# Kernel optimization log

Hardware: AMD Instinct MI355X
Metric: run time of the kernel (lower is better)

The kernel has to match this reference:

```python
import jax, jax.numpy as jnp
import numpy as np

BS, T, H = 4, 2048, 512
N_HEAD = 8
D_HEAD = H // N_HEAD  # 64


def setup_inputs() -> dict:
    key = jax.random.key(0)
    k1, k2, k3 = jax.random.split(key, 3)
    x = jax.random.normal(k1, (BS, T, H), dtype=jnp.float32)
    # torch Linear(hidden, (2*n_head+1)*d_head) -> store transposed for x @ W
    w_qkv = jax.random.normal(k2, (H, (2 * N_HEAD + 1) * D_HEAD), dtype=jnp.float32) * (H ** -0.5)
    w_out = jax.random.normal(k3, (D_HEAD, H), dtype=jnp.float32) * (D_HEAD ** -0.5)
    return {"x": x, "w_qkv": w_qkv, "w_out": w_out}


def reference(x, w_qkv, w_out):
    bs, t, h = x.shape
    n_head, d_head = N_HEAD, D_HEAD
    scale = d_head ** -0.5

    qkv = x @ w_qkv  # [bs, t, (2*n_head+1)*d_head]
    q, k, v = jnp.split(qkv, [n_head * d_head, 2 * n_head * d_head], axis=-1)
    q = q.reshape(bs, t, n_head, d_head)
    k = k.reshape(bs, t, n_head, d_head)
    # v stays [bs, t, d_head]: a single V shared across all heads

    # causal mask: -inf strictly above the diagonal
    mask = jnp.triu(jnp.full((t, t), -jnp.inf, dtype=x.dtype), 1)

    # scores: [bs, n_head, t_q, t_k]
    attn_score = jnp.einsum('bqhd,bkhd->bhqk', q, k) * scale + mask
    attn_prob = jax.nn.softmax(attn_score, axis=-1)

    # shared V broadcast over heads: [bs, n_head, t, d_head]
    attn_vec = jnp.einsum('bhqk,bkd->bhqd', attn_prob, v)
    m_attn_vec = jnp.mean(attn_vec, axis=1)  # mean over heads -> [bs, t, d_head]

    out = m_attn_vec @ w_out  # [bs, t, hidden]
    return out, attn_prob
```

## Files before the change

### kernel.cpp

```cpp
#include <hip/hip_runtime.h>

typedef unsigned short u16;
typedef __bf16 bf16x8 __attribute__((ext_vector_type(8)));
typedef float f32x4 __attribute__((ext_vector_type(4)));
static_assert(sizeof(bf16x8) == 16, "bf16x8 must be 16B");

#define MFMA(a, b, c) __builtin_amdgcn_mfma_f32_16x16x32_bf16(a, b, c, 0, 0, 0)

__device__ __forceinline__ u16 f2bf(float f) {
  unsigned u = __float_as_uint(f);
  u += 0x7fffu + ((u >> 16) & 1u);
  return (u16)(u >> 16);
}

__global__ __launch_bounds__(256) void prep_kernel(
    const float* __restrict__ x, const float* __restrict__ wqkv,
    const float* __restrict__ wout, u16* __restrict__ xh,
    u16* __restrict__ wt, u16* __restrict__ wot) {
  int blk = blockIdx.x, tid = threadIdx.x;
  if (blk < 4096) {
    int idx = (blk * 256 + tid) * 4;
    float4 v = *(const float4*)(x + idx);
    ushort4 o;
    o.x = f2bf(v.x); o.y = f2bf(v.y); o.z = f2bf(v.z); o.w = f2bf(v.w);
    *(ushort4*)(xh + idx) = o;
  } else if (blk < 4096 + 2176) {
    int idx = (blk - 4096) * 256 + tid;
    int n = idx >> 9, k = idx & 511;
    float v = wqkv[k * 1088 + n];
    if (n < 512) v *= 0.125f;
    wt[idx] = f2bf(v);
  } else {
    int idx = (blk - 6272) * 256 + tid;
    int n = idx >> 6, d = idx & 63;
    wot[idx] = f2bf(wout[d * 512 + n]);
  }
}

__global__ __launch_bounds__(256) void qkv_gemm_kernel(
    const u16* __restrict__ xh, const u16* __restrict__ wt,
    u16* __restrict__ Qb, u16* __restrict__ Kb, u16* __restrict__ Vt) {
  __shared__ u16 As[128][40];
  __shared__ u16 Bs[64][40];
  const int tid = threadIdx.x;
  const int w = tid >> 6, l = tid & 63, g = l >> 4, c16 = l & 15;
  const int n0 = blockIdx.x * 64;
  const int m0 = blockIdx.y * 128;
  const int arow = tid >> 1, acol = (tid & 1) << 4;
  const int brow = tid >> 2, bcol = (tid & 3) << 3;
  const u16* ap = xh + (size_t)(m0 + arow) * 512 + acol;
  const u16* bp = wt + (size_t)(n0 + brow) * 512 + bcol;
  uint4 pa0 = *(const uint4*)(ap);
  uint4 pa1 = *(const uint4*)(ap + 8);
  uint4 pb0 = *(const uint4*)(bp);
  f32x4 acc[2][4] = {};
  for (int k0 = 0; k0 < 512; k0 += 32) {
    __syncthreads();
    *(uint4*)&As[arow][acol] = pa0;
    *(uint4*)&As[arow][acol + 8] = pa1;
    *(uint4*)&Bs[brow][bcol] = pb0;
    __syncthreads();
    if (k0 + 32 < 512) {
      pa0 = *(const uint4*)(ap + k0 + 32);
      pa1 = *(const uint4*)(ap + k0 + 40);
      pb0 = *(const uint4*)(bp + k0 + 32);
    }
#pragma unroll
    for (int mt = 0; mt < 2; ++mt) {
      bf16x8 a = *(const bf16x8*)&As[w * 32 + mt * 16 + c16][g * 8];
#pragma unroll
      for (int nt = 0; nt < 4; ++nt) {
        bf16x8 b = *(const bf16x8*)&Bs[nt * 16 + c16][g * 8];
        acc[mt][nt] = MFMA(a, b, acc[mt][nt]);
      }
    }
  }
#pragma unroll
  for (int mt = 0; mt < 2; ++mt)
#pragma unroll
    for (int nt = 0; nt < 4; ++nt)
#pragma unroll
      for (int j = 0; j < 4; ++j) {
        u16 bv = f2bf(acc[mt][nt][j]);
        int row = m0 + w * 32 + mt * 16 + g * 4 + j;
        int b = row >> 11, t = row & 2047;
        int col = n0 + nt * 16 + c16;
        if (col < 512) {
          int h = col >> 6, d = col & 63;
          Qb[((size_t)((b << 3) + h) * 2048 + t) * 64 + d] = bv;
        } else if (col < 1024) {
          int cc = col - 512, h = cc >> 6, d = cc & 63;
          Kb[((size_t)((b << 3) + h) * 2048 + t) * 64 + d] = bv;
        } else {
          int d = col - 1024;
          Vt[((size_t)((b << 6) + d)) * 2048 + t] = bv;
        }
      }
}

__global__ __launch_bounds__(256) void attn_kernel(
    const u16* __restrict__ Qb, const u16* __restrict__ Kb,
    const u16* __restrict__ Vt, float* __restrict__ P,
    float* __restrict__ Obuf) {
  __shared__ u16 Ps[64][72];
  __shared__ u16 Ks[2][64][72];
  const int tid = threadIdx.x;
  const int w = tid >> 6, l = tid & 63, g = l >> 4, c16 = l & 15;
  const int bidx = blockIdx.x;
  const int ii = bidx >> 5, jj = bidx & 31;
  const int qt = ((ii >> 3) & 1) ? (31 - jj) : jj;
  const int bh = ii, b = bh >> 3;
  const int srow = tid >> 2, scol = (tid & 3) << 4;

  const u16* qrow = Qb + ((size_t)(bh * 2048 + qt * 64 + w * 16 + c16)) * 64;
  const bf16x8 aq0 = *(const bf16x8*)(qrow + g * 8);
  const bf16x8 aq1 = *(const bf16x8*)(qrow + 32 + g * 8);

  const u16* kb = Kb + ((size_t)bh * 2048) * 64;
  const u16* vb = Vt + ((size_t)(b << 6)) * 2048;

  float lsum = 0.f;

  uint4 ka0 = *(const uint4*)(kb + (size_t)srow * 64 + scol);
  uint4 ka1 = *(const uint4*)(kb + (size_t)srow * 64 + scol + 8);
  for (int kt = 0; kt <= qt; ++kt) {
    const int cur = kt & 1;
    *(uint4*)&Ks[cur][srow][scol] = ka0;
    *(uint4*)&Ks[cur][srow][scol + 8] = ka1;
    if (kt < qt) {
      const u16* kn = kb + (size_t)((kt + 1) * 64 + srow) * 64 + scol;
      ka0 = *(const uint4*)(kn);
      ka1 = *(const uint4*)(kn + 8);
    }
    __syncthreads();
    f32x4 st[4];
    __builtin_amdgcn_s_setprio(1);
#pragma unroll
    for (int nt = 0; nt < 4; ++nt) {
      bf16x8 k0 = *(const bf16x8*)&Ks[cur][nt * 16 + c16][g * 8];
      bf16x8 k1 = *(const bf16x8*)&Ks[cur][nt * 16 + c16][32 + g * 8];
      f32x4 a = {};
      a = MFMA(k0, aq0, a);
      a = MFMA(k1, aq1, a);
      st[nt] = a;
    }
    __builtin_amdgcn_s_setprio(0);
    if (kt == qt) {
#pragma unroll
      for (int nt = 0; nt < 4; ++nt)
#pragma unroll
        for (int j = 0; j < 4; ++j)
          if (nt * 16 + g * 4 + j > w * 16 + c16) st[nt][j] = -3.0e38f;
    }
#pragma unroll
    for (int nt = 0; nt < 4; ++nt)
#pragma unroll
      for (int j = 0; j < 4; ++j) lsum += __expf(st[nt][j]);
  }
  lsum += __shfl_xor(lsum, 16, 64);
  lsum += __shfl_xor(lsum, 32, 64);
  const float rl = 1.0f / lsum;

  __syncthreads();

  f32x4 oacc[4] = {};
  ka0 = *(const uint4*)(kb + (size_t)srow * 64 + scol);
  ka1 = *(const uint4*)(kb + (size_t)srow * 64 + scol + 8);
  float* prow = P +
      ((size_t)(bh * 2048 + qt * 64 + w * 16 + c16)) * 2048 + g * 4;
  for (int kt = 0; kt <= qt; ++kt) {
    const int cur = kt & 1;
    *(uint4*)&Ks[cur][srow][scol] = ka0;
    *(uint4*)&Ks[cur][srow][scol + 8] = ka1;
    if (kt < qt) {
      const u16* kn = kb + (size_t)((kt + 1) * 64 + srow) * 64 + scol;
      ka0 = *(const uint4*)(kn);
      ka1 = *(const uint4*)(kn + 8);
    }
    __syncthreads();
    f32x4 st[4];
    __builtin_amdgcn_s_setprio(1);
#pragma unroll
    for (int nt = 0; nt < 4; ++nt) {
      bf16x8 k0 = *(const bf16x8*)&Ks[cur][nt * 16 + c16][g * 8];
      bf16x8 k1 = *(const bf16x8*)&Ks[cur][nt * 16 + c16][32 + g * 8];
      f32x4 a = {};
      a = MFMA(k0, aq0, a);
      a = MFMA(k1, aq1, a);
      st[nt] = a;
    }
    __builtin_amdgcn_s_setprio(0);
    bf16x8 v0[4], v1[4];
#pragma unroll
    for (int nt = 0; nt < 4; ++nt) {
      const u16* vr = vb + (size_t)(nt * 16 + c16) * 2048 + kt * 64 + g * 8;
      v0[nt] = *(const bf16x8*)(vr);
      v1[nt] = *(const bf16x8*)(vr + 32);
    }
    if (kt == qt) {
#pragma unroll
      for (int nt = 0; nt < 4; ++nt)
#pragma unroll
        for (int j = 0; j < 4; ++j)
          if (nt * 16 + g * 4 + j > w * 16 + c16) st[nt][j] = -3.0e38f;
    }
#pragma unroll
    for (int nt = 0; nt < 4; ++nt) {
      f32x4 pv;
#pragma unroll
      for (int j = 0; j < 4; ++j) pv[j] = __expf(st[nt][j]) * rl;
      __builtin_nontemporal_store(
          pv, (f32x4*)(prow + (size_t)kt * 64 + nt * 16));
      unsigned r0, r1;
      asm("v_cvt_pk_bf16_f32 %0, %1, %2" : "=v"(r0) : "v"(pv[0]), "v"(pv[1]));
      asm("v_cvt_pk_bf16_f32 %0, %1, %2" : "=v"(r1) : "v"(pv[2]), "v"(pv[3]));
      uint2 pk; pk.x = r0; pk.y = r1;
      *(uint2*)&Ps[w * 16 + c16][nt * 16 + g * 4] = pk;
    }
    bf16x8 ap0 = *(const bf16x8*)&Ps[w * 16 + c16][g * 8];
    bf16x8 ap1 = *(const bf16x8*)&Ps[w * 16 + c16][32 + g * 8];
    __builtin_amdgcn_s_setprio(1);
#pragma unroll
    for (int nt = 0; nt < 4; ++nt) {
      oacc[nt] = MFMA(ap0, v0[nt], oacc[nt]);
      oacc[nt] = MFMA(ap1, v1[nt], oacc[nt]);
    }
    __builtin_amdgcn_s_setprio(0);
  }

  {
    float* obase = Obuf + ((size_t)(bh * 2048 + qt * 64 + w * 16)) * 64;
#pragma unroll
    for (int nt = 0; nt < 4; ++nt)
#pragma unroll
      for (int j = 0; j < 4; ++j)
        obase[(g * 4 + j) * 64 + nt * 16 + c16] = oacc[nt][j];
  }
  {
    int colstart = (qt + 1) * 64;
    int nf4 = (2048 - colstart) >> 2;
    float* base = P + ((size_t)(bh * 2048 + qt * 64)) * 2048;
    f32x4 z = {0.f, 0.f, 0.f, 0.f};
    for (int r = 0; r < 64; ++r) {
      f32x4* rowp = (f32x4*)(base + (size_t)r * 2048 + colstart);
      for (int u = tid; u < nf4; u += 256)
        __builtin_nontemporal_store(z, rowp + u);
    }
  }
}

__global__ __launch_bounds__(256) void mean_kernel(
    const float* __restrict__ Obuf, u16* __restrict__ meanb) {
  int o4 = blockIdx.x * 256 + threadIdx.x;
  int d4 = o4 & 15, t = (o4 >> 4) & 2047, b = o4 >> 15;
  f32x4 acc = {0.f, 0.f, 0.f, 0.f};
#pragma unroll
  for (int h = 0; h < 8; ++h) {
    f32x4 v = *(const f32x4*)(Obuf +
        ((size_t)((b << 3) + h) * 2048 + t) * 64 + d4 * 4);
    acc += v;
  }
  ushort4 o;
  o.x = f2bf(acc[0] * 0.125f); o.y = f2bf(acc[1] * 0.125f);
  o.z = f2bf(acc[2] * 0.125f); o.w = f2bf(acc[3] * 0.125f);
  *(ushort4*)(meanb + (size_t)o4 * 4) = o;
}

__global__ __launch_bounds__(256) void out_gemm_kernel(
    const u16* __restrict__ meanb, const u16* __restrict__ wot,
    float* __restrict__ out) {
  __shared__ u16 As[64][72];
  __shared__ u16 Bs[64][72];
  const int tid = threadIdx.x;
  const int w = tid >> 6, l = tid & 63, g = l >> 4, c16 = l & 15;
  const int n0 = blockIdx.x * 64;
  const int m0 = blockIdx.y * 64;
  const int srow = tid >> 2, scol = (tid & 3) << 4;
  {
    const u16* asrc = meanb + (size_t)(m0 + srow) * 64 + scol;
    *(uint4*)&As[srow][scol] = *(const uint4*)(asrc);
    *(uint4*)&As[srow][scol + 8] = *(const uint4*)(asrc + 8);
    const u16* bsrc = wot + (size_t)(n0 + srow) * 64 + scol;
    *(uint4*)&Bs[srow][scol] = *(const uint4*)(bsrc);
    *(uint4*)&Bs[srow][scol + 8] = *(const uint4*)(bsrc + 8);
  }
  __syncthreads();
  bf16x8 a0 = *(const bf16x8*)&As[w * 16 + c16][g * 8];
  bf16x8 a1 = *(const bf16x8*)&As[w * 16 + c16][32 + g * 8];
  f32x4 acc[4] = {};
#pragma unroll
  for (int nt = 0; nt < 4; ++nt) {
    bf16x8 b0 = *(const bf16x8*)&Bs[nt * 16 + c16][g * 8];
    bf16x8 b1 = *(const bf16x8*)&Bs[nt * 16 + c16][32 + g * 8];
    acc[nt] = MFMA(a0, b0, acc[nt]);
    acc[nt] = MFMA(a1, b1, acc[nt]);
  }
#pragma unroll
  for (int nt = 0; nt < 4; ++nt)
#pragma unroll
    for (int j = 0; j < 4; ++j)
      __builtin_nontemporal_store(
          acc[nt][j],
          out + (size_t)(m0 + w * 16 + g * 4 + j) * 512 + n0 + nt * 16 + c16);
}

extern "C" void kernel_launch(void* const* d_in, const int* in_sizes, int n_in,
                              void* d_out, int out_size, void* d_ws,
                              size_t ws_size, hipStream_t stream) {
  (void)in_sizes; (void)n_in; (void)out_size; (void)ws_size;
  const float* x = (const float*)d_in[0];
  const float* wqkv = (const float*)d_in[1];
  const float* wout = (const float*)d_in[2];
  float* out = (float*)d_out;
  float* P = out + 4194304;

  u16* xh = (u16*)d_ws;
  u16* wt = xh + 4194304;
  u16* wot = wt + 557056;
  u16* Qb = wot + 32768;
  u16* Kb = Qb + 4194304;
  u16* Vt = Kb + 4194304;
  float* Obuf = (float*)(Vt + 524288);
  u16* meanb = xh;

  hipLaunchKernelGGL(prep_kernel, dim3(6400), dim3(256), 0, stream,
                     x, wqkv, wout, xh, wt, wot);
  hipLaunchKernelGGL(qkv_gemm_kernel, dim3(17, 64), dim3(256), 0, stream,
                     xh, wt, Qb, Kb, Vt);
  hipLaunchKernelGGL(attn_kernel, dim3(1024), dim3(256), 0, stream,
                     Qb, Kb, Vt, P, Obuf);
  hipLaunchKernelGGL(mean_kernel, dim3(512), dim3(256), 0, stream,
                     Obuf, meanb);
  hipLaunchKernelGGL(out_gemm_kernel, dim3(8, 128), dim3(256), 0, stream,
                     meanb, wot, out);
}
```

Measured before the change: 649.2 us.

## Enlarge attention query tile to 128 rows with 512-thread blocks

The attention kernel now handles 128 query rows per block using 8 waves and 512 threads, so each K tile staged in shared memory serves twice as many queries. The grid is halved, and causal masking now covers the last two key tiles using absolute indices. The intent is to cut redundant K loads and block overhead. In exchange, causal work per block becomes more uneven, up to 64 fully masked keys per row are computed on the diagonal tiles, and occupancy changes with the 512-thread launch bounds.

```diff
diff --git a/kernel.cpp b/kernel.cpp
--- a/kernel.cpp
+++ b/kernel.cpp
@@ -98,21 +98,24 @@
       }
 }
 
-__global__ __launch_bounds__(256) void attn_kernel(
+__global__ __launch_bounds__(512, 4) void attn_kernel(
     const u16* __restrict__ Qb, const u16* __restrict__ Kb,
     const u16* __restrict__ Vt, float* __restrict__ P,
     float* __restrict__ Obuf) {
-  __shared__ u16 Ps[64][72];
+  __shared__ u16 Ps[128][72];
   __shared__ u16 Ks[2][64][72];
   const int tid = threadIdx.x;
   const int w = tid >> 6, l = tid & 63, g = l >> 4, c16 = l & 15;
   const int bidx = blockIdx.x;
-  const int ii = bidx >> 5, jj = bidx & 31;
-  const int qt = ((ii >> 3) & 1) ? (31 - jj) : jj;
+  const int ii = bidx >> 4, jj = bidx & 15;
+  const int qt = ((ii >> 4) & 1) ? (15 - jj) : jj;
   const int bh = ii, b = bh >> 3;
-  const int srow = tid >> 2, scol = (tid & 3) << 4;
-
-  const u16* qrow = Qb + ((size_t)(bh * 2048 + qt * 64 + w * 16 + c16)) * 64;
+  const int srow = tid >> 3, scol = (tid & 7) << 3;
+  const int ql = w * 16 + c16;
+  const int qg = qt * 128 + ql;
+  const int nkt = 2 * qt + 2;
+
+  const u16* qrow = Qb + ((size_t)(bh * 2048 + qg)) * 64;
   const bf16x8 aq0 = *(const bf16x8*)(qrow + g * 8);
   const bf16x8 aq1 = *(const bf16x8*)(qrow + 32 + g * 8);
 
@@ -121,17 +124,12 @@
 
   float lsum = 0.f;
 
-  uint4 ka0 = *(const uint4*)(kb + (size_t)srow * 64 + scol);
-  uint4 ka1 = *(const uint4*)(kb + (size_t)srow * 64 + scol + 8);
-  for (int kt = 0; kt <= qt; ++kt) {
+  uint4 ka = *(const uint4*)(kb + (size_t)srow * 64 + scol);
+  for (int kt = 0; kt < nkt; ++kt) {
     const int cur = kt & 1;
-    *(uint4*)&Ks[cur][srow][scol] = ka0;
-    *(uint4*)&Ks[cur][srow][scol + 8] = ka1;
-    if (kt < qt) {
-      const u16* kn = kb + (size_t)((kt + 1) * 64 + srow) * 64 + scol;
-      ka0 = *(const uint4*)(kn);
-      ka1 = *(const uint4*)(kn + 8);
-    }
+    *(uint4*)&Ks[cur][srow][scol] = ka;
+    if (kt + 1 < nkt)
+      ka = *(const uint4*)(kb + (size_t)((kt + 1) * 64 + srow) * 64 + scol);
     __syncthreads();
     f32x4 st[4];
     __builtin_amdgcn_s_setprio(1);
@@ -145,12 +143,12 @@
       st[nt] = a;
     }
     __builtin_amdgcn_s_setprio(0);
-    if (kt == qt) {
+    if (kt >= 2 * qt) {
 #pragma unroll
       for (int nt = 0; nt < 4; ++nt)
 #pragma unroll
         for (int j = 0; j < 4; ++j)
-          if (nt * 16 + g * 4 + j > w * 16 + c16) st[nt][j] = -3.0e38f;
+          if (kt * 64 + nt * 16 + g * 4 + j > qg) st[nt][j] = -3.0e38f;
     }
 #pragma unroll
     for (int nt = 0; nt < 4; ++nt)
@@ -164,19 +162,13 @@
   __syncthreads();
 
   f32x4 oacc[4] = {};
-  ka0 = *(const uint4*)(kb + (size_t)srow * 64 + scol);
-  ka1 = *(const uint4*)(kb + (size_t)srow * 64 + scol + 8);
-  float* prow = P +
-      ((size_t)(bh * 2048 + qt * 64 + w * 16 + c16)) * 2048 + g * 4;
-  for (int kt = 0; kt <= qt; ++kt) {
+  ka = *(const uint4*)(kb + (size_t)srow * 64 + scol);
+  float* prow = P + ((size_t)(bh * 2048 + qg)) * 2048 + g * 4;
+  for (int kt = 0; kt < nkt; ++kt) {
     const int cur = kt & 1;
-    *(uint4*)&Ks[cur][srow][scol] = ka0;
-    *(uint4*)&Ks[cur][srow][scol + 8] = ka1;
-    if (kt < qt) {
-      const u16* kn = kb + (size_t)((kt + 1) * 64 + srow) * 64 + scol;
-      ka0 = *(const uint4*)(kn);
-      ka1 = *(const uint4*)(kn + 8);
-    }
+    *(uint4*)&Ks[cur][srow][scol] = ka;
+    if (kt + 1 < nkt)
+      ka = *(const uint4*)(kb + (size_t)((kt + 1) * 64 + srow) * 64 + scol);
     __syncthreads();
     f32x4 st[4];
     __builtin_amdgcn_s_setprio(1);
@@ -197,12 +189,12 @@
       v0[nt] = *(const bf16x8*)(vr);
       v1[nt] = *(const bf16x8*)(vr + 32);
     }
-    if (kt == qt) {
+    if (kt >= 2 * qt) {
 #pragma unroll
       for (int nt = 0; nt < 4; ++nt)
 #pragma unroll
         for (int j = 0; j < 4; ++j)
-          if (nt * 16 + g * 4 + j > w * 16 + c16) st[nt][j] = -3.0e38f;
+          if (kt * 64 + nt * 16 + g * 4 + j > qg) st[nt][j] = -3.0e38f;
     }
 #pragma unroll
     for (int nt = 0; nt < 4; ++nt) {
@@ -215,10 +207,10 @@
       asm("v_cvt_pk_bf16_f32 %0, %1, %2" : "=v"(r0) : "v"(pv[0]), "v"(pv[1]));
       asm("v_cvt_pk_bf16_f32 %0, %1, %2" : "=v"(r1) : "v"(pv[2]), "v"(pv[3]));
       uint2 pk; pk.x = r0; pk.y = r1;
-      *(uint2*)&Ps[w * 16 + c16][nt * 16 + g * 4] = pk;
-    }
-    bf16x8 ap0 = *(const bf16x8*)&Ps[w * 16 + c16][g * 8];
-    bf16x8 ap1 = *(const bf16x8*)&Ps[w * 16 + c16][32 + g * 8];
+      *(uint2*)&Ps[ql][nt * 16 + g * 4] = pk;
+    }
+    bf16x8 ap0 = *(const bf16x8*)&Ps[ql][g * 8];
+    bf16x8 ap1 = *(const bf16x8*)&Ps[ql][32 + g * 8];
     __builtin_amdgcn_s_setprio(1);
 #pragma unroll
     for (int nt = 0; nt < 4; ++nt) {
@@ -229,7 +221,7 @@
   }
 
   {
-    float* obase = Obuf + ((size_t)(bh * 2048 + qt * 64 + w * 16)) * 64;
+    float* obase = Obuf + ((size_t)(bh * 2048 + qt * 128 + w * 16)) * 64;
 #pragma unroll
     for (int nt = 0; nt < 4; ++nt)
 #pragma unroll
@@ -237,13 +229,13 @@
         obase[(g * 4 + j) * 64 + nt * 16 + c16] = oacc[nt][j];
   }
   {
-    int colstart = (qt + 1) * 64;
+    int colstart = nkt * 64;
     int nf4 = (2048 - colstart) >> 2;
-    float* base = P + ((size_t)(bh * 2048 + qt * 64)) * 2048;
+    float* base = P + ((size_t)(bh * 2048 + qt * 128)) * 2048;
     f32x4 z = {0.f, 0.f, 0.f, 0.f};
-    for (int r = 0; r < 64; ++r) {
+    for (int r = 0; r < 128; ++r) {
       f32x4* rowp = (f32x4*)(base + (size_t)r * 2048 + colstart);
-      for (int u = tid; u < nf4; u += 256)
+      for (int u = tid; u < nf4; u += 512)
         __builtin_nontemporal_store(z, rowp + u);
     }
   }
@@ -327,7 +319,7 @@
                      x, wqkv, wout, xh, wt, wot);
   hipLaunchKernelGGL(qkv_gemm_kernel, dim3(17, 64), dim3(256), 0, stream,
                      xh, wt, Qb, Kb, Vt);
-  hipLaunchKernelGGL(attn_kernel, dim3(1024), dim3(256), 0, stream,
+  hipLaunchKernelGGL(attn_kernel, dim3(512), dim3(512), 0, stream,
                      Qb, Kb, Vt, P, Obuf);
   hipLaunchKernelGGL(mean_kernel, dim3(512), dim3(256), 0, stream,
                      Obuf, meanb);
```

Measured after the change: 671.6 us. 1.03x slower.
